# Kernel optimization log

Hardware: AMD Instinct MI355X
Metric: run time of the kernel (lower is better)

Reference implementation:

```python
import jax, jax.numpy as jnp
import numpy as np


def _bin_ids(start, length, S, P):
    # For adaptive max pool, output bin i over a region of length L covers
    # [floor(i*L/P), ceil((i+1)*L/P)). Adjacent bins overlap by at most one
    # element (when L >= P), so element h belongs to bins A(h)..B(h) with
    #   A(h) = floor(h*P/L),  B(h) = ceil((h+1)*P/L) - 1,  B - A <= 1.
    # Out-of-region positions are dumped into segment P.
    pos = jnp.arange(S, dtype=start.dtype)               # (S,)
    local = pos[None, :] - start[:, None]                # (N, S) local coord
    L = length[:, None]                                  # (N, 1)
    valid = (local >= 0) & (local < L)
    idA = jnp.where(valid, (local * P) // L, P)
    idB = jnp.where(valid, -((-((local + 1) * P)) // L) - 1, P)
    return idA, idB


def _roi_pool(feature_map, rois, PH, PW):
    C, H, W = feature_map.shape
    y, x, rH, rW = rois[:, 0], rois[:, 1], rois[:, 2], rois[:, 3]

    # ---- pool rows: (C,H,W) -> (N, PH, C, W) ----
    idA_h, idB_h = _bin_ids(y, rH, H, PH)                # (N, H) each
    fm_hcw = jnp.transpose(feature_map, (1, 0, 2))       # (H, C, W)
    seg_h = lambda ids: jax.ops.segment_max(fm_hcw, ids, num_segments=PH + 1)
    pooled_h = jnp.maximum(jax.vmap(seg_h)(idA_h), jax.vmap(seg_h)(idB_h))[:, :PH]

    # ---- pool cols: (N, PH, C, W) -> (N, PW, PH, C) ----
    idA_w, idB_w = _bin_ids(x, rW, W, PW)                # (N, W) each
    data_w = jnp.transpose(pooled_h, (0, 3, 1, 2))       # (N, W, PH, C)
    seg_w = lambda d, ids: jax.ops.segment_max(d, ids, num_segments=PW + 1)
    pooled = jnp.maximum(jax.vmap(seg_w)(data_w, idA_w),
                         jax.vmap(seg_w)(data_w, idB_w))[:, :PW]
    return jnp.transpose(pooled, (0, 3, 2, 1))           # (N, C, PH, PW)


def setup_inputs() -> dict:
    key = jax.random.key(0)
    k1, k2, k3, k4, k5 = jax.random.split(key, 5)
    C, H, W, N, PH, PW = 256, 128, 128, 256, 8, 8
    feature_map = jax.random.normal(k1, (C, H, W), dtype=jnp.float32)
    # valid ROIs: rH >= PH, rW >= PW, fully in-bounds
    rH = jax.random.randint(k2, (N,), PH, H + 1, dtype=jnp.int32)
    rW = jax.random.randint(k3, (N,), PW, W + 1, dtype=jnp.int32)
    y = (jax.random.uniform(k4, (N,)) * (H - rH + 1).astype(jnp.float32)).astype(jnp.int32)
    x = (jax.random.uniform(k5, (N,)) * (W - rW + 1).astype(jnp.float32)).astype(jnp.int32)
    rois = jnp.stack([y, x, rH, rW], axis=1)
    return {"feature_map": feature_map, "rois": rois, "PH": PH, "PW": PW}


def reference(feature_map, rois, PH, PW):
    return _roi_pool(feature_map, rois, PH, PW)
```

## Files before the change

kernel.cpp:

```cpp
#include <hip/hip_runtime.h>
#include <math.h>

#define C_ 256
#define H_ 128
#define W_ 128
#define PH_ 8
#define PW_ 8
#define HW_ (H_ * W_)

typedef unsigned short u16;
typedef u16 u16x4 __attribute__((ext_vector_type(4)));
typedef u16 u16x8 __attribute__((ext_vector_type(8)));

__device__ __forceinline__ u16x8 kmax(u16x8 a, u16x8 b) {
    return __builtin_elementwise_max(a, b);
}

__device__ __forceinline__ u16 f32_to_key(float f) {
    unsigned u = __float_as_uint(f);
    unsigned r = (u + 0x7fffu + ((u >> 16) & 1u)) >> 16;
    u16 b = (u16)r;
    return (b & 0x8000u) ? (u16)~b : (u16)(b | 0x8000u);
}
__device__ __forceinline__ float key_to_f32(u16 k) {
    u16 b = (k & 0x8000u) ? (u16)(k & 0x7fffu) : (u16)~k;
    return __uint_as_float(((unsigned)b) << 16);
}

__global__ __launch_bounds__(256) void transpose_kernel(
    const float* __restrict__ fm, u16* __restrict__ fmt, u16* __restrict__ pmax)
{
    __shared__ float tile[32 * 257];
    const int tid = threadIdx.x;
    const int g   = blockIdx.x & 7;
    const int hwb = blockIdx.x >> 3;
    const int c0  = g * 32;
    const int hw0 = hwb * 256;

    const int l    = tid & 63;
    const int crow = tid >> 6;
    const int sw   = (l >> 3) & 3;
    #pragma unroll
    for (int k = 0; k < 8; ++k) {
        const int c = crow + 4 * k;
        const float4 v = *(const float4*)(fm + (size_t)(c0 + c) * HW_ + hw0 + 4 * l);
        float* t = tile + c * 257 + 4 * l;
        t[(0 + sw) & 3] = v.x;
        t[(1 + sw) & 3] = v.y;
        t[(2 + sw) & 3] = v.z;
        t[(3 + sw) & 3] = v.w;
    }
    __syncthreads();

    u16* dst = fmt + (size_t)g * HW_ * 32;
    const int cq  = tid & 7;
    const int hwr = tid >> 3;
    #pragma unroll
    for (int m = 0; m < 8; ++m) {
        const int hw = hwr + 32 * m;
        const int o  = (hw & ~3) | (((hw & 3) + m) & 3);
        u16x4 w;
        w.x = f32_to_key(tile[(4 * cq + 0) * 257 + o]);
        w.y = f32_to_key(tile[(4 * cq + 1) * 257 + o]);
        w.z = f32_to_key(tile[(4 * cq + 2) * 257 + o]);
        w.w = f32_to_key(tile[(4 * cq + 3) * 257 + o]);
        *(u16x4*)(dst + (size_t)(hw0 + hw) * 32 + 4 * cq) = w;
    }

    u16* pdst = pmax + (size_t)g * (HW_ / 2) * 32;
    #pragma unroll
    for (int m = 0; m < 4; ++m) {
        const int w_ = hwr + 32 * m;
        const int o  = (w_ & ~3) | (((w_ & 3) + m) & 3);
        u16x4 v;
        v.x = f32_to_key(fmaxf(tile[(4 * cq + 0) * 257 + o],
                               tile[(4 * cq + 0) * 257 + o + 128]));
        v.y = f32_to_key(fmaxf(tile[(4 * cq + 1) * 257 + o],
                               tile[(4 * cq + 1) * 257 + o + 128]));
        v.z = f32_to_key(fmaxf(tile[(4 * cq + 2) * 257 + o],
                               tile[(4 * cq + 2) * 257 + o + 128]));
        v.w = f32_to_key(fmaxf(tile[(4 * cq + 3) * 257 + o],
                               tile[(4 * cq + 3) * 257 + o + 128]));
        *(u16x4*)(pdst + ((size_t)hwb * W_ + w_) * 32 + 4 * cq) = v;
    }
}

__global__ __launch_bounds__(256) void pool_kernel(
    const u16* __restrict__ fmt, const u16* __restrict__ pmax,
    const int* __restrict__ rois, float* __restrict__ out, int N)
{
    const int bid  = blockIdx.x;
    const int cg   = bid & 7;
    const int phh  = (bid >> 3) & 1;
    const int half = (bid >> 4) & 1;
    const int n    = bid >> 5;

    const int wid  = threadIdx.x >> 6;
    const int lane = threadIdx.x & 63;
    const int pw   = half * 4 + wid;
    const int pg   = lane >> 2;
    const int co   = (lane & 3) << 3;

    const int4 roi = ((const int4*)rois)[n];
    const int y = roi.x, x = roi.y, rH = roi.z, rW = roi.w;

    const int ws = (pw * rW) >> 3;
    const int we = ((pw + 1) * rW + 7) >> 3;
    const int bw = we - ws;
    const int nsteps = (bw + 15) >> 4;

    const u16* plane  = fmt  + (size_t)cg * HW_ * 32;
    const u16* pplane = pmax + (size_t)cg * (HW_ / 2) * 32;
    const size_t RS = (size_t)W_ * 32;

    #pragma unroll
    for (int pj = 0; pj < 4; ++pj) {
        const int ph = phh * 4 + pj;
        const int hs = (ph * rH) >> 3;
        const int he = ((ph + 1) * rH + 7) >> 3;
        const int a  = y + hs;
        const int b  = y + he;
        const int k0 = (a + 1) >> 1;
        const int k1 = b >> 1;
        const int np = k1 - k0;

        u16x8 acc = {0, 0, 0, 0, 0, 0, 0, 0};

        for (int s = 0; s < nsteps; ++s) {
            const int col = ws + 16 * s + pg;
            if (col < we) {
                const size_t cofs = (size_t)(x + col) * 32 + co;
                if (a & 1)
                    acc = kmax(acc, *(const u16x8*)(plane + (size_t)a * RS + cofs));
                if (b & 1)
                    acc = kmax(acc, *(const u16x8*)(plane + (size_t)(b - 1) * RS + cofs));
                if (np > 0) {
                    const u16* pp = pplane + (size_t)k0 * RS + cofs;
                    const int last = np - 1;
                    if (np <= 4) {
                        u16x8 t0 = *(const u16x8*)(pp);
                        u16x8 t1 = *(const u16x8*)(pp + (size_t)min(1, last) * RS);
                        u16x8 t2 = *(const u16x8*)(pp + (size_t)min(2, last) * RS);
                        u16x8 t3 = *(const u16x8*)(pp + (size_t)min(3, last) * RS);
                        acc = kmax(acc, kmax(kmax(t0, t1), kmax(t2, t3)));
                    } else {
                        u16x8 t0 = *(const u16x8*)(pp);
                        u16x8 t1 = *(const u16x8*)(pp + RS);
                        u16x8 t2 = *(const u16x8*)(pp + 2 * RS);
                        u16x8 t3 = *(const u16x8*)(pp + 3 * RS);
                        u16x8 t4 = *(const u16x8*)(pp + 4 * RS);
                        u16x8 t5 = *(const u16x8*)(pp + (size_t)min(5, last) * RS);
                        u16x8 t6 = *(const u16x8*)(pp + (size_t)min(6, last) * RS);
                        u16x8 t7 = *(const u16x8*)(pp + (size_t)min(7, last) * RS);
                        t0 = kmax(t0, t1); t2 = kmax(t2, t3);
                        t4 = kmax(t4, t5); t6 = kmax(t6, t7);
                        acc = kmax(acc, kmax(kmax(t0, t2), kmax(t4, t6)));
                    }
                }
            }
        }

        union U { u16x8 v; unsigned u[4]; };
        U aa; aa.v = acc;
        #pragma unroll
        for (int mask = 4; mask <= 32; mask <<= 1) {
            U t;
            #pragma unroll
            for (int i = 0; i < 4; ++i) t.u[i] = __shfl_xor(aa.u[i], mask, 64);
            aa.v = __builtin_elementwise_max(aa.v, t.v);
        }

        if (pg == 0) {
            const int c = (cg << 5) + co;
            float* o = out + ((size_t)n * C_ + c) * (PH_ * PW_) + ph * PW_ + pw;
            #pragma unroll
            for (int i = 0; i < 8; ++i)
                o[(size_t)i * (PH_ * PW_)] = key_to_f32(aa.v[i]);
        }
    }
}

__global__ __launch_bounds__(256) void roi_pool_fallback(
    const float* __restrict__ fm, const int* __restrict__ rois,
    float* __restrict__ out, int N)
{
    const int wid  = threadIdx.x >> 6;
    const int lane = threadIdx.x & 63;
    const int bid  = blockIdx.x;
    const int xcd  = bid & 7;
    const int t    = bid >> 3;
    const int csub = t & 7;
    const int n    = t >> 3;
    if (n >= N) return;
    const int c = (xcd << 5) + (csub << 2) + wid;

    const int4 roi = ((const int4*)rois)[n];
    const int y = roi.x, x = roi.y, rH = roi.z, rW = roi.w;

    const float2* plane2 = (const float2*)(fm + (size_t)c * (H_ * W_));
    const int pw = lane & 7;
    const int j  = lane >> 3;
    const int ws = (pw * rW) >> 3;
    const int we = (((pw + 1) * rW) + 7) >> 3;

    #pragma unroll
    for (int ph = 0; ph < PH_; ++ph) {
        const int hs = (ph * rH) >> 3;
        const int he = ((ph + 1) * rH + 7) >> 3;
        const float2* p = plane2 + (size_t)(y + hs) * (W_ / 2) + lane;
        float m0 = -INFINITY, m1 = -INFINITY;
        int cnt = he - hs;
        while (cnt >= 2) {
            const float2 a = p[0];
            const float2 b = p[W_ / 2];
            p += W_; cnt -= 2;
            m0 = fmaxf(m0, fmaxf(a.x, b.x));
            m1 = fmaxf(m1, fmaxf(a.y, b.y));
        }
        if (cnt) { const float2 a = p[0]; m0 = fmaxf(m0, a.x); m1 = fmaxf(m1, a.y); }

        float rr = -INFINITY;
        #pragma unroll
        for (int k = 0; k < 3; ++k) {
            const int w  = ws + j + k * 8;
            const int wa = x + w;
            const float a = __shfl(m0, (wa >> 1) & 63, 64);
            const float b = __shfl(m1, (wa >> 1) & 63, 64);
            if (w < we) rr = fmaxf(rr, (wa & 1) ? b : a);
        }
        rr = fmaxf(rr, __shfl_xor(rr, 8, 64));
        rr = fmaxf(rr, __shfl_xor(rr, 16, 64));
        rr = fmaxf(rr, __shfl_xor(rr, 32, 64));
        if (lane < PW_) out[(((size_t)n * C_ + c) * PH_ + ph) * PW_ + lane] = rr;
    }
}

extern "C" void kernel_launch(void* const* d_in, const int* in_sizes, int n_in,
                              void* d_out, int out_size, void* d_ws, size_t ws_size,
                              hipStream_t stream) {
    const float* fm   = (const float*)d_in[0];
    const int*   rois = (const int*)d_in[1];
    float*       out  = (float*)d_out;
    const int N = in_sizes[1] / 4;

    const size_t fmt_bytes  = (size_t)HW_ * C_ * sizeof(u16);
    const size_t pmax_bytes = (size_t)(HW_ / 2) * C_ * sizeof(u16);
    if (ws_size >= fmt_bytes + pmax_bytes) {
        u16* fmt = (u16*)d_ws;
        u16* pmx = (u16*)((char*)d_ws + fmt_bytes);
        transpose_kernel<<<dim3((HW_ / 256) * 8), 256, 0, stream>>>(fm, fmt, pmx);
        pool_kernel<<<dim3(N * 32), 256, 0, stream>>>(fmt, pmx, rois, out, N);
    } else {
        roi_pool_fallback<<<dim3(64 * N), 256, 0, stream>>>(fm, rois, out, N);
    }
}
```

Baseline: 118.9 us.

## Replace row-pair max table with 8-row sliding-window max table

Drops the pairwise row-max table built inside the transpose kernel. A new kernel instead builds a table where each entry is the max over 8 consecutive rows. The pool kernel then covers any bin of 8 to 17 rows with two overlapping window loads, plus one plain row load when the bin has 17 rows, and falls back to direct row loads for shorter bins. This is meant to cut the number of global loads per bin. In exchange it adds a third kernel launch with only 64 blocks and a larger workspace (121 rows instead of 64) that must be written and then read back.

```diff
diff --git a/kernel.cpp b/kernel.cpp
--- a/kernel.cpp
+++ b/kernel.cpp
@@ -7,6 +7,7 @@
 #define PH_ 8
 #define PW_ 8
 #define HW_ (H_ * W_)
+#define M3ROWS (H_ - 8 + 1)
 
 typedef unsigned short u16;
 typedef u16 u16x4 __attribute__((ext_vector_type(4)));
@@ -28,7 +29,7 @@
 }
 
 __global__ __launch_bounds__(256) void transpose_kernel(
-    const float* __restrict__ fm, u16* __restrict__ fmt, u16* __restrict__ pmax)
+    const float* __restrict__ fm, u16* __restrict__ fmt)
 {
     __shared__ float tile[32 * 257];
     const int tid = threadIdx.x;
@@ -66,27 +67,49 @@
         w.w = f32_to_key(tile[(4 * cq + 3) * 257 + o]);
         *(u16x4*)(dst + (size_t)(hw0 + hw) * 32 + 4 * cq) = w;
     }
-
-    u16* pdst = pmax + (size_t)g * (HW_ / 2) * 32;
-    #pragma unroll
-    for (int m = 0; m < 4; ++m) {
-        const int w_ = hwr + 32 * m;
-        const int o  = (w_ & ~3) | (((w_ & 3) + m) & 3);
-        u16x4 v;
-        v.x = f32_to_key(fmaxf(tile[(4 * cq + 0) * 257 + o],
-                               tile[(4 * cq + 0) * 257 + o + 128]));
-        v.y = f32_to_key(fmaxf(tile[(4 * cq + 1) * 257 + o],
-                               tile[(4 * cq + 1) * 257 + o + 128]));
-        v.z = f32_to_key(fmaxf(tile[(4 * cq + 2) * 257 + o],
-                               tile[(4 * cq + 2) * 257 + o + 128]));
-        v.w = f32_to_key(fmaxf(tile[(4 * cq + 3) * 257 + o],
-                               tile[(4 * cq + 3) * 257 + o + 128]));
-        *(u16x4*)(pdst + ((size_t)hwb * W_ + w_) * 32 + 4 * cq) = v;
+}
+
+__global__ __launch_bounds__(256) void m3_kernel(
+    const u16* __restrict__ fmt, u16* __restrict__ m3)
+{
+    const int bid  = blockIdx.x;
+    const int g    = bid & 7;
+    const int band = bid >> 3;
+    const int i0   = band * 16;
+    const int t    = threadIdx.x;
+    const int co   = (t & 3) << 3;
+    const int w0   = t >> 2;
+
+    const u16* src = fmt + (size_t)g * HW_ * 32;
+    u16*       dst = m3  + (size_t)g * M3ROWS * (W_ * 32);
+    const size_t RS = (size_t)W_ * 32;
+
+    #pragma unroll 1
+    for (int seg = 0; seg < 2; ++seg) {
+        const int w = w0 + 64 * seg;
+        const size_t cofs = (size_t)w * 32 + co;
+        u16x8 r[8];
+        #pragma unroll
+        for (int k = 0; k < 7; ++k)
+            r[k] = *(const u16x8*)(src + (size_t)(i0 + k) * RS + cofs);
+        #pragma unroll
+        for (int j = 0; j < 16; ++j) {
+            const int i = i0 + j;
+            if (i < M3ROWS) {
+                r[(j + 7) & 7] = *(const u16x8*)(src + (size_t)(i + 7) * RS + cofs);
+                u16x8 m01 = kmax(r[0], r[1]);
+                u16x8 m23 = kmax(r[2], r[3]);
+                u16x8 m45 = kmax(r[4], r[5]);
+                u16x8 m67 = kmax(r[6], r[7]);
+                *(u16x8*)(dst + (size_t)i * RS + cofs) =
+                    kmax(kmax(m01, m23), kmax(m45, m67));
+            }
+        }
     }
 }
 
 __global__ __launch_bounds__(256) void pool_kernel(
-    const u16* __restrict__ fmt, const u16* __restrict__ pmax,
+    const u16* __restrict__ fmt, const u16* __restrict__ m3,
     const int* __restrict__ rois, float* __restrict__ out, int N)
 {
     const int bid  = blockIdx.x;
@@ -109,8 +132,8 @@
     const int bw = we - ws;
     const int nsteps = (bw + 15) >> 4;
 
-    const u16* plane  = fmt  + (size_t)cg * HW_ * 32;
-    const u16* pplane = pmax + (size_t)cg * (HW_ / 2) * 32;
+    const u16* plane   = fmt + (size_t)cg * HW_ * 32;
+    const u16* m3plane = m3  + (size_t)cg * M3ROWS * (W_ * 32);
     const size_t RS = (size_t)W_ * 32;
 
     #pragma unroll
@@ -120,9 +143,7 @@
         const int he = ((ph + 1) * rH + 7) >> 3;
         const int a  = y + hs;
         const int b  = y + he;
-        const int k0 = (a + 1) >> 1;
-        const int k1 = b >> 1;
-        const int np = k1 - k0;
+        const int L  = he - hs;
 
         u16x8 acc = {0, 0, 0, 0, 0, 0, 0, 0};
 
@@ -130,32 +151,32 @@
             const int col = ws + 16 * s + pg;
             if (col < we) {
                 const size_t cofs = (size_t)(x + col) * 32 + co;
-                if (a & 1)
-                    acc = kmax(acc, *(const u16x8*)(plane + (size_t)a * RS + cofs));
-                if (b & 1)
-                    acc = kmax(acc, *(const u16x8*)(plane + (size_t)(b - 1) * RS + cofs));
-                if (np > 0) {
-                    const u16* pp = pplane + (size_t)k0 * RS + cofs;
-                    const int last = np - 1;
-                    if (np <= 4) {
-                        u16x8 t0 = *(const u16x8*)(pp);
-                        u16x8 t1 = *(const u16x8*)(pp + (size_t)min(1, last) * RS);
-                        u16x8 t2 = *(const u16x8*)(pp + (size_t)min(2, last) * RS);
-                        u16x8 t3 = *(const u16x8*)(pp + (size_t)min(3, last) * RS);
-                        acc = kmax(acc, kmax(kmax(t0, t1), kmax(t2, t3)));
-                    } else {
-                        u16x8 t0 = *(const u16x8*)(pp);
-                        u16x8 t1 = *(const u16x8*)(pp + RS);
-                        u16x8 t2 = *(const u16x8*)(pp + 2 * RS);
-                        u16x8 t3 = *(const u16x8*)(pp + 3 * RS);
-                        u16x8 t4 = *(const u16x8*)(pp + 4 * RS);
-                        u16x8 t5 = *(const u16x8*)(pp + (size_t)min(5, last) * RS);
-                        u16x8 t6 = *(const u16x8*)(pp + (size_t)min(6, last) * RS);
-                        u16x8 t7 = *(const u16x8*)(pp + (size_t)min(7, last) * RS);
-                        t0 = kmax(t0, t1); t2 = kmax(t2, t3);
-                        t4 = kmax(t4, t5); t6 = kmax(t6, t7);
-                        acc = kmax(acc, kmax(kmax(t0, t2), kmax(t4, t6)));
-                    }
+                if (L >= 8) {
+                    u16x8 t0 = *(const u16x8*)(m3plane + (size_t)a * RS + cofs);
+                    u16x8 t1 = *(const u16x8*)(m3plane + (size_t)(b - 8) * RS + cofs);
+                    acc = kmax(acc, kmax(t0, t1));
+                    if (L > 16)
+                        acc = kmax(acc, *(const u16x8*)(plane + (size_t)(a + 8) * RS + cofs));
+                } else if (L > 4) {
+                    const u16* pp = plane + (size_t)a * RS + cofs;
+                    const int last = L - 1;
+                    u16x8 t0 = *(const u16x8*)(pp);
+                    u16x8 t1 = *(const u16x8*)(pp + RS);
+                    u16x8 t2 = *(const u16x8*)(pp + 2 * RS);
+                    u16x8 t3 = *(const u16x8*)(pp + 3 * RS);
+                    u16x8 t4 = *(const u16x8*)(pp + 4 * RS);
+                    u16x8 t5 = *(const u16x8*)(pp + (size_t)min(5, last) * RS);
+                    u16x8 t6 = *(const u16x8*)(pp + (size_t)min(6, last) * RS);
+                    acc = kmax(acc, kmax(kmax(kmax(t0, t1), kmax(t2, t3)),
+                                         kmax(kmax(t4, t5), t6)));
+                } else {
+                    const u16* pp = plane + (size_t)a * RS + cofs;
+                    const int last = L - 1;
+                    u16x8 t0 = *(const u16x8*)(pp);
+                    u16x8 t1 = *(const u16x8*)(pp + (size_t)min(1, last) * RS);
+                    u16x8 t2 = *(const u16x8*)(pp + (size_t)min(2, last) * RS);
+                    u16x8 t3 = *(const u16x8*)(pp + (size_t)min(3, last) * RS);
+                    acc = kmax(acc, kmax(kmax(t0, t1), kmax(t2, t3)));
                 }
             }
         }
@@ -243,13 +264,14 @@
     float*       out  = (float*)d_out;
     const int N = in_sizes[1] / 4;
 
-    const size_t fmt_bytes  = (size_t)HW_ * C_ * sizeof(u16);
-    const size_t pmax_bytes = (size_t)(HW_ / 2) * C_ * sizeof(u16);
-    if (ws_size >= fmt_bytes + pmax_bytes) {
+    const size_t fmt_bytes = (size_t)HW_ * C_ * sizeof(u16);
+    const size_t m3_bytes  = (size_t)M3ROWS * W_ * C_ * sizeof(u16);
+    if (ws_size >= fmt_bytes + m3_bytes) {
         u16* fmt = (u16*)d_ws;
-        u16* pmx = (u16*)((char*)d_ws + fmt_bytes);
-        transpose_kernel<<<dim3((HW_ / 256) * 8), 256, 0, stream>>>(fm, fmt, pmx);
-        pool_kernel<<<dim3(N * 32), 256, 0, stream>>>(fmt, pmx, rois, out, N);
+        u16* m3  = (u16*)((char*)d_ws + fmt_bytes);
+        transpose_kernel<<<dim3((HW_ / 256) * 8), 256, 0, stream>>>(fm, fmt);
+        m3_kernel<<<dim3(64), 256, 0, stream>>>(fmt, m3);
+        pool_kernel<<<dim3(N * 32), 256, 0, stream>>>(fmt, m3, rois, out, N);
     } else {
         roi_pool_fallback<<<dim3(64 * N), 256, 0, stream>>>(fm, rois, out, N);
     }
```

Result: no change. 118.4 us (-0.5%).
